# Kernel tuning notes

Hardware: AMD Instinct MI355X
Metric: run time of the kernel (lower is better)

Reference implementation:

```python
import jax, jax.numpy as jnp
import numpy as np

B, L, DIM = 2, 4096, 512
HEADS, KS = 8, 33
HEAD_DIM = DIM // HEADS
SCALE = HEAD_DIM ** -0.5


def setup_inputs() -> dict:
    key = jax.random.key(0)
    ks = jax.random.split(key, 5)
    s = 0.02
    return {
        "x": jax.random.normal(ks[0], (B, L, DIM), dtype=jnp.float32),
        "w_qkv": jax.random.normal(ks[1], (3 * DIM, DIM), dtype=jnp.float32) * s,
        "b_qkv": jax.random.normal(ks[2], (3 * DIM,), dtype=jnp.float32) * s,
        "w_proj": jax.random.normal(ks[3], (DIM, DIM), dtype=jnp.float32) * s,
        "b_proj": jax.random.normal(ks[4], (DIM,), dtype=jnp.float32) * s,
    }


def _na1d(q, k, v):
    # q,k,v: [B, L, H, d]. Each query i attends to KS tokens whose window
    # start is clamp(i - KS//2, 0, L-KS) (NATTEN boundary-clamped neighborhood).
    starts = jnp.clip(jnp.arange(L) - KS // 2, 0, L - KS)          # [L]
    idx = starts[:, None] + jnp.arange(KS)[None, :]                # [L, KS]
    k_g = k[:, idx]                                                # [B, L, KS, H, d]
    v_g = v[:, idx]                                                # [B, L, KS, H, d]
    scores = jnp.einsum("blhd,blkhd->bhlk", q * SCALE, k_g)        # [B, H, L, KS]
    attn = jax.nn.softmax(scores, axis=-1)
    out = jnp.einsum("bhlk,blkhd->blhd", attn, v_g)                # [B, L, H, d]
    return out


def reference(x, w_qkv, b_qkv, w_proj, b_proj):
    qkv = x @ w_qkv.T + b_qkv                                      # [B, L, 3*DIM]
    qkv = qkv.reshape(B, L, 3, HEADS, HEAD_DIM)
    q, k, v = qkv[:, :, 0], qkv[:, :, 1], qkv[:, :, 2]
    out = _na1d(q, k, v).reshape(B, L, DIM)
    return out @ w_proj.T + b_proj
```

## Files before the change

kernel.cpp:

```cpp
#include <hip/hip_runtime.h>
#include <hip/hip_bf16.h>

#define B_ 2
#define L_ 4096
#define DIM_ 512
#define HEADS_ 8
#define HDIM_ 64
#define KS_ 33
#define QKS_ 1024

typedef __bf16 bf16;
typedef __bf16 bf16x4 __attribute__((ext_vector_type(4)));
typedef __bf16 bf16x8 __attribute__((ext_vector_type(8)));
typedef float f32x4 __attribute__((ext_vector_type(4)));

typedef __attribute__((address_space(3))) void lds_void;
typedef __attribute__((address_space(1))) const void glb_void;

__device__ __forceinline__ void async_cp16(const bf16* g, bf16* l)
{
    __builtin_amdgcn_global_load_lds((glb_void*)g, (lds_void*)l, 16, 0, 0);
}

__global__ __launch_bounds__(256)
void cvt_all(const float* __restrict__ x,  const float* __restrict__ wq,
             const float* __restrict__ bq, const float* __restrict__ wp,
             const float* __restrict__ bp,
             bf16* __restrict__ xb,  bf16* __restrict__ wqb,
             bf16* __restrict__ bqb, bf16* __restrict__ wpb,
             bf16* __restrict__ bpb)
{
    const int blk = blockIdx.x;
    const float* src; bf16* dst; int n, base;
    if (blk < 2048)       { src = x;  dst = xb;  n = 4194304; base = blk; }
    else if (blk < 2432)  { src = wq; dst = wqb; n = 786432;  base = blk - 2048; }
    else if (blk < 2560)  { src = wp; dst = wpb; n = 262144;  base = blk - 2432; }
    else if (blk == 2560) { src = bq; dst = bqb; n = 1536;    base = 0; }
    else                  { src = bp; dst = bpb; n = 512;     base = 0; }
    int i = base * 2048 + threadIdx.x * 8;
    if (i + 8 <= n) {
        float4 a = *(const float4*)(src + i);
        float4 b = *(const float4*)(src + i + 4);
        bf16x8 o;
        o[0] = (bf16)a.x; o[1] = (bf16)a.y; o[2] = (bf16)a.z; o[3] = (bf16)a.w;
        o[4] = (bf16)b.x; o[5] = (bf16)b.y; o[6] = (bf16)b.z; o[7] = (bf16)b.w;
        *(bf16x8*)(dst + i) = o;
    }
}

#define GEMM_CORE(A_, W_, K_)                                                  \
    __shared__ bf16 As[128][64];                                               \
    __shared__ bf16 Bs[64][64];                                                \
    const int tid  = threadIdx.x;                                              \
    const int wave = tid >> 6;                                                 \
    const int lane = tid & 63;                                                 \
    const int wm   = (wave >> 1) * 64;                                         \
    const int wn   = (wave & 1) * 32;                                          \
    const int l16  = lane & 15;                                                \
    const int quad = lane >> 4;                                                \
    const int row0 = blockIdx.x * 128;                                         \
    const int col0 = blockIdx.y * 64;                                          \
    f32x4 acc[4][2] = {};                                                      \
    for (int k0 = 0; k0 < (K_); k0 += 64) {                                    \
        _Pragma("unroll")                                                      \
        for (int it = 0; it < 6; ++it) {                                       \
            int f = it * 256 + tid;                                            \
            if (f < 1024) {                                                    \
                int r = f >> 3, pc = f & 7, lc = pc ^ (r & 7);                 \
                async_cp16(&(A_)[(size_t)(row0 + r) * (K_) + k0 + lc * 8],     \
                           &As[r][pc * 8]);                                    \
            } else {                                                           \
                int g = f - 1024;                                              \
                int r = g >> 3, pc = g & 7, lc = pc ^ (r & 7);                 \
                async_cp16(&(W_)[(size_t)(col0 + r) * (K_) + k0 + lc * 8],     \
                           &Bs[r][pc * 8]);                                    \
            }                                                                  \
        }                                                                      \
        __syncthreads();                                                       \
        _Pragma("unroll")                                                      \
        for (int ks = 0; ks < 2; ++ks) {                                       \
            bf16x8 af[4], bfr[2];                                              \
            _Pragma("unroll")                                                  \
            for (int i = 0; i < 4; ++i) {                                      \
                int ra = wm + i * 16 + l16;                                    \
                af[i] = *(const bf16x8*)(&As[ra][((ks * 4 + quad) ^ (ra & 7)) * 8]); \
            }                                                                  \
            _Pragma("unroll")                                                  \
            for (int i = 0; i < 2; ++i) {                                      \
                int rb = wn + i * 16 + l16;                                    \
                bfr[i] = *(const bf16x8*)(&Bs[rb][((ks * 4 + quad) ^ (rb & 7)) * 8]); \
            }                                                                  \
            _Pragma("unroll")                                                  \
            for (int mi = 0; mi < 4; ++mi)                                     \
                _Pragma("unroll")                                              \
                for (int ni = 0; ni < 2; ++ni)                                 \
                    acc[mi][ni] = __builtin_amdgcn_mfma_f32_16x16x32_bf16(     \
                        af[mi], bfr[ni], acc[mi][ni], 0, 0, 0);                \
        }                                                                      \
        __syncthreads();                                                       \
    }

__global__ __launch_bounds__(256)
void gemm_qkv(const bf16* __restrict__ A, const bf16* __restrict__ W,
              const bf16* __restrict__ bias,
              bf16* __restrict__ qk, bf16* __restrict__ vT)
{
    GEMM_CORE(A, W, DIM_)

    if (col0 < 1024) {
        #pragma unroll
        for (int ni = 0; ni < 2; ++ni) {
            int n = col0 + wn + ni * 16 + l16;
            float bv = (float)bias[n];
            #pragma unroll
            for (int mi = 0; mi < 4; ++mi) {
                int mrow = row0 + wm + mi * 16 + quad * 4;
                #pragma unroll
                for (int r = 0; r < 4; ++r)
                    qk[(size_t)(mrow + r) * QKS_ + n] = (bf16)(acc[mi][ni][r] + bv);
            }
        }
    } else {
        #pragma unroll
        for (int ni = 0; ni < 2; ++ni) {
            int nf = col0 + wn + ni * 16 + l16;
            float bv = (float)bias[nf];
            int hd = nf - 1024;
            #pragma unroll
            for (int mi = 0; mi < 4; ++mi) {
                int m = row0 + wm + mi * 16 + quad * 4;
                int b = m >> 12;
                int l = m & (L_ - 1);
                bf16x4 v4;
                #pragma unroll
                for (int r = 0; r < 4; ++r) v4[r] = (bf16)(acc[mi][ni][r] + bv);
                *(bf16x4*)(vT + ((size_t)(b * DIM_ + hd)) * L_ + l) = v4;
            }
        }
    }
}

__global__ __launch_bounds__(256)
void gemm_proj(const bf16* __restrict__ A, const bf16* __restrict__ W,
               const bf16* __restrict__ bias, float* __restrict__ C)
{
    GEMM_CORE(A, W, DIM_)

    #pragma unroll
    for (int ni = 0; ni < 2; ++ni) {
        int n = col0 + wn + ni * 16 + l16;
        float bv = (float)bias[n];
        #pragma unroll
        for (int mi = 0; mi < 4; ++mi) {
            int mrow = row0 + wm + mi * 16 + quad * 4;
            #pragma unroll
            for (int r = 0; r < 4; ++r)
                C[(size_t)(mrow + r) * DIM_ + n] = acc[mi][ni][r] + bv;
        }
    }
}

__global__ __launch_bounds__(256)
void na1d_attn_mfma(const bf16* __restrict__ qk, const bf16* __restrict__ vT,
                    bf16* __restrict__ att)
{
    __shared__ bf16 Klds[96 * 64];
    __shared__ bf16 Plds[4][16][72];

    const int tid  = threadIdx.x;
    const int wave = tid >> 6;
    const int lane = tid & 63;
    const int l16  = lane & 15;
    const int quad = lane >> 4;

    const int xcd  = blockIdx.x & 7;
    const int s    = blockIdx.x >> 3;
    const int jj   = s & 3;
    const int half = (s >> 2) & 1;
    const int h    = (s >> 3) & 7;
    const int b    = s >> 6;
    const int p    = jj * 8 + xcd;
    const int Q0   = p * 128 + half * 64;

    const size_t rowbase = (size_t)b * L_;

    #pragma unroll
    for (int i = 0; i < 3; ++i) {
        int ck = i * 256 + tid;
        int r  = ck >> 3;
        int pc = ck & 7;
        int lc = pc ^ (r & 7);
        int g  = Q0 - 16 + r;
        g = g < 0 ? 0 : (g > L_ - 1 ? L_ - 1 : g);
        async_cp16(qk + (rowbase + g) * QKS_ + DIM_ + h * HDIM_ + lc * 8,
                   Klds + (size_t)ck * 8);
    }

    const int q0w = Q0 + wave * 16;
    const bf16* qptr = qk + (rowbase + q0w + l16) * QKS_ + h * HDIM_ + quad * 8;
    bf16x8 qf0 = *(const bf16x8*)(qptr);
    bf16x8 qf1 = *(const bf16x8*)(qptr + 32);

    int k_base = q0w - 16;
    if (k_base > L_ - 48) k_base = L_ - 48;
    if (k_base < 0) k_base = 0;
    const int rel = k_base - (Q0 - 16);

    __syncthreads();

    f32x4 sacc[3] = {};
    #pragma unroll
    for (int t = 0; t < 3; ++t) {
        int r = rel + t * 16 + l16;
        bf16x8 kf0 = *(const bf16x8*)(Klds + r * 64 + ((quad ^ (r & 7)) * 8));
        bf16x8 kf1 = *(const bf16x8*)(Klds + r * 64 + (((4 + quad) ^ (r & 7)) * 8));
        sacc[t] = __builtin_amdgcn_mfma_f32_16x16x32_bf16(qf0, kf0, sacc[t], 0, 0, 0);
        sacc[t] = __builtin_amdgcn_mfma_f32_16x16x32_bf16(qf1, kf1, sacc[t], 0, 0, 0);
    }

    int offr[4];
    #pragma unroll
    for (int r = 0; r < 4; ++r) {
        int lq = q0w + quad * 4 + r;
        int st = lq - KS_ / 2;
        if (st < 0) st = 0;
        if (st > L_ - KS_) st = L_ - KS_;
        offr[r] = st - k_base;
    }
    float sv[3][4];
    #pragma unroll
    for (int t = 0; t < 3; ++t) {
        int j = t * 16 + l16;
        #pragma unroll
        for (int r = 0; r < 4; ++r) {
            float xv = sacc[t][r] * 0.125f;
            sv[t][r] = (j >= offr[r] && j <= offr[r] + 32) ? xv : -1e30f;
        }
    }

    float mr[4], sum[4];
    #pragma unroll
    for (int r = 0; r < 4; ++r)
        mr[r] = fmaxf(fmaxf(sv[0][r], sv[1][r]), sv[2][r]);
    #pragma unroll
    for (int o = 1; o < 16; o <<= 1)
        #pragma unroll
        for (int r = 0; r < 4; ++r)
            mr[r] = fmaxf(mr[r], __shfl_xor(mr[r], o, 64));
    #pragma unroll
    for (int t = 0; t < 3; ++t)
        #pragma unroll
        for (int r = 0; r < 4; ++r)
            sv[t][r] = __expf(sv[t][r] - mr[r]);
    #pragma unroll
    for (int r = 0; r < 4; ++r)
        sum[r] = sv[0][r] + sv[1][r] + sv[2][r];
    #pragma unroll
    for (int o = 1; o < 16; o <<= 1)
        #pragma unroll
        for (int r = 0; r < 4; ++r)
            sum[r] += __shfl_xor(sum[r], o, 64);
    #pragma unroll
    for (int r = 0; r < 4; ++r) {
        float inv = 1.0f / sum[r];
        #pragma unroll
        for (int t = 0; t < 3; ++t) sv[t][r] *= inv;
    }

    bf16* P = &Plds[wave][0][0];
    {
        int rr = lane >> 2;
        int c0 = 48 + (lane & 3) * 4;
        *(bf16x4*)(&P[rr * 72 + c0]) = (bf16x4){(bf16)0.f, (bf16)0.f, (bf16)0.f, (bf16)0.f};
    }
    #pragma unroll
    for (int t = 0; t < 3; ++t)
        #pragma unroll
        for (int r = 0; r < 4; ++r)
            P[(quad * 4 + r) * 72 + t * 16 + l16] = (bf16)sv[t][r];
    __syncthreads();

    bf16x8 pf0 = *(const bf16x8*)(&P[l16 * 72 + quad * 8]);
    bf16x8 pf1 = *(const bf16x8*)(&P[l16 * 72 + 32 + quad * 8]);

    const bf16* vbase = vT + (size_t)(b * DIM_ + h * HDIM_) * L_;
    int c1 = k_base + quad * 8;
    int c2 = k_base + 32 + quad * 8;
    if (c2 > L_ - 8) c2 = L_ - 8;
    f32x4 o[4] = {};
    #pragma unroll
    for (int t = 0; t < 4; ++t) {
        const bf16* vrow = vbase + (size_t)(t * 16 + l16) * L_;
        bf16x8 vf0 = *(const bf16x8*)(vrow + c1);
        bf16x8 vf1 = *(const bf16x8*)(vrow + c2);
        o[t] = __builtin_amdgcn_mfma_f32_16x16x32_bf16(pf0, vf0, o[t], 0, 0, 0);
        o[t] = __builtin_amdgcn_mfma_f32_16x16x32_bf16(pf1, vf1, o[t], 0, 0, 0);
    }

    bf16* orow = att + (rowbase + q0w) * DIM_ + h * HDIM_;
    #pragma unroll
    for (int t = 0; t < 4; ++t)
        #pragma unroll
        for (int r = 0; r < 4; ++r)
            orow[(size_t)(quad * 4 + r) * DIM_ + t * 16 + l16] = (bf16)o[t][r];
}

extern "C" void kernel_launch(void* const* d_in, const int* in_sizes, int n_in,
                              void* d_out, int out_size, void* d_ws, size_t ws_size,
                              hipStream_t stream) {
    const int n_x  = B_ * L_ * DIM_;
    const int n_wq = 3 * DIM_ * DIM_;
    const int n_bq = 3 * DIM_;
    const int n_wp = DIM_ * DIM_;
    const int n_bp = DIM_;

    char* ws = (char*)d_ws;
    bf16* xb  = (bf16*)ws;
    bf16* wqb = xb  + n_x;
    bf16* bqb = wqb + n_wq;
    bf16* wpb = bqb + n_bq;
    bf16* bpb = wpb + n_wp;
    bf16* qk  = bpb + n_bp;
    bf16* vT  = qk  + (size_t)8192 * 1024;
    bf16* att = vT  + (size_t)B_ * DIM_ * L_;

    float* out = (float*)d_out;
    const int M = B_ * L_;

    cvt_all<<<2562, 256, 0, stream>>>(
        (const float*)d_in[0], (const float*)d_in[1], (const float*)d_in[2],
        (const float*)d_in[3], (const float*)d_in[4],
        xb, wqb, bqb, wpb, bpb);

    gemm_qkv<<<dim3(M / 128, (3 * DIM_) / 64), 256, 0, stream>>>(
        xb, wqb, bqb, qk, vT);

    na1d_attn_mfma<<<dim3((B_ * HEADS_ * L_) / 64), 256, 0, stream>>>(qk, vT, att);

    gemm_proj<<<dim3(M / 128, DIM_ / 64), 256, 0, stream>>>(
        att, wpb, bpb, out);
}
```

Before: 118.0 us.

## Load GEMM fragments directly from global and shrink attention blocks to 32 queries

The GEMM core drops LDS staging and barriers and has each wave load its MFMA fragments straight from global memory, relying on L1/L2 caching for reuse across waves. The attention kernel moves from 64-query, 256-thread blocks to 32-query, 128-thread blocks with a smaller K tile in LDS, doubling the grid. The aim is to cut synchronisation and LDS overhead and raise block count. The cost is more redundant global traffic and uncoalesced 16-byte row loads in the GEMMs, plus more K-halo reloads per query in attention.

```diff
diff --git a/kernel.cpp b/kernel.cpp
--- a/kernel.cpp
+++ b/kernel.cpp
@@ -48,9 +48,7 @@
     }
 }
 
-#define GEMM_CORE(A_, W_, K_)                                                  \
-    __shared__ bf16 As[128][64];                                               \
-    __shared__ bf16 Bs[64][64];                                                \
+#define DGEMM_CORE(A_, W_, K_)                                                 \
     const int tid  = threadIdx.x;                                              \
     const int wave = tid >> 6;                                                 \
     const int lane = tid & 63;                                                 \
@@ -60,44 +58,24 @@
     const int quad = lane >> 4;                                                \
     const int row0 = blockIdx.x * 128;                                         \
     const int col0 = blockIdx.y * 64;                                          \
+    const bf16* Ap = (A_) + (size_t)(row0 + wm + l16) * (K_) + quad * 8;       \
+    const bf16* Wp = (W_) + (size_t)(col0 + wn + l16) * (K_) + quad * 8;       \
     f32x4 acc[4][2] = {};                                                      \
-    for (int k0 = 0; k0 < (K_); k0 += 64) {                                    \
+    _Pragma("unroll 4")                                                        \
+    for (int k = 0; k < (K_); k += 32) {                                       \
+        bf16x8 af[4], bfr[2];                                                  \
         _Pragma("unroll")                                                      \
-        for (int it = 0; it < 6; ++it) {                                       \
-            int f = it * 256 + tid;                                            \
-            if (f < 1024) {                                                    \
-                int r = f >> 3, pc = f & 7, lc = pc ^ (r & 7);                 \
-                async_cp16(&(A_)[(size_t)(row0 + r) * (K_) + k0 + lc * 8],     \
-                           &As[r][pc * 8]);                                    \
-            } else {                                                           \
-                int g = f - 1024;                                              \
-                int r = g >> 3, pc = g & 7, lc = pc ^ (r & 7);                 \
-                async_cp16(&(W_)[(size_t)(col0 + r) * (K_) + k0 + lc * 8],     \
-                           &Bs[r][pc * 8]);                                    \
-            }                                                                  \
-        }                                                                      \
-        __syncthreads();                                                       \
+        for (int i = 0; i < 4; ++i)                                            \
+            af[i] = *(const bf16x8*)(Ap + (size_t)i * 16 * (K_) + k);          \
         _Pragma("unroll")                                                      \
-        for (int ks = 0; ks < 2; ++ks) {                                       \
-            bf16x8 af[4], bfr[2];                                              \
+        for (int i = 0; i < 2; ++i)                                            \
+            bfr[i] = *(const bf16x8*)(Wp + (size_t)i * 16 * (K_) + k);         \
+        _Pragma("unroll")                                                      \
+        for (int mi = 0; mi < 4; ++mi)                                         \
             _Pragma("unroll")                                                  \
-            for (int i = 0; i < 4; ++i) {                                      \
-                int ra = wm + i * 16 + l16;                                    \
-                af[i] = *(const bf16x8*)(&As[ra][((ks * 4 + quad) ^ (ra & 7)) * 8]); \
-            }                                                                  \
-            _Pragma("unroll")                                                  \
-            for (int i = 0; i < 2; ++i) {                                      \
-                int rb = wn + i * 16 + l16;                                    \
-                bfr[i] = *(const bf16x8*)(&Bs[rb][((ks * 4 + quad) ^ (rb & 7)) * 8]); \
-            }                                                                  \
-            _Pragma("unroll")                                                  \
-            for (int mi = 0; mi < 4; ++mi)                                     \
-                _Pragma("unroll")                                              \
-                for (int ni = 0; ni < 2; ++ni)                                 \
-                    acc[mi][ni] = __builtin_amdgcn_mfma_f32_16x16x32_bf16(     \
-                        af[mi], bfr[ni], acc[mi][ni], 0, 0, 0);                \
-        }                                                                      \
-        __syncthreads();                                                       \
+            for (int ni = 0; ni < 2; ++ni)                                     \
+                acc[mi][ni] = __builtin_amdgcn_mfma_f32_16x16x32_bf16(         \
+                    af[mi], bfr[ni], acc[mi][ni], 0, 0, 0);                    \
     }
 
 __global__ __launch_bounds__(256)
@@ -105,7 +83,7 @@
               const bf16* __restrict__ bias,
               bf16* __restrict__ qk, bf16* __restrict__ vT)
 {
-    GEMM_CORE(A, W, DIM_)
+    DGEMM_CORE(A, W, DIM_)
 
     if (col0 < 1024) {
         #pragma unroll
@@ -144,7 +122,7 @@
 void gemm_proj(const bf16* __restrict__ A, const bf16* __restrict__ W,
                const bf16* __restrict__ bias, float* __restrict__ C)
 {
-    GEMM_CORE(A, W, DIM_)
+    DGEMM_CORE(A, W, DIM_)
 
     #pragma unroll
     for (int ni = 0; ni < 2; ++ni) {
@@ -160,12 +138,12 @@
     }
 }
 
-__global__ __launch_bounds__(256)
+__global__ __launch_bounds__(128)
 void na1d_attn_mfma(const bf16* __restrict__ qk, const bf16* __restrict__ vT,
                     bf16* __restrict__ att)
 {
-    __shared__ bf16 Klds[96 * 64];
-    __shared__ bf16 Plds[4][16][72];
+    __shared__ bf16 Klds[64 * 64];
+    __shared__ bf16 Plds[2][16][72];
 
     const int tid  = threadIdx.x;
     const int wave = tid >> 6;
@@ -175,18 +153,18 @@
 
     const int xcd  = blockIdx.x & 7;
     const int s    = blockIdx.x >> 3;
-    const int jj   = s & 3;
-    const int half = (s >> 2) & 1;
-    const int h    = (s >> 3) & 7;
-    const int b    = s >> 6;
+    const int qtr  = s & 3;
+    const int jj   = (s >> 2) & 3;
+    const int h    = (s >> 4) & 7;
+    const int b    = s >> 7;
     const int p    = jj * 8 + xcd;
-    const int Q0   = p * 128 + half * 64;
+    const int Q0   = p * 128 + qtr * 32;
 
     const size_t rowbase = (size_t)b * L_;
 
     #pragma unroll
-    for (int i = 0; i < 3; ++i) {
-        int ck = i * 256 + tid;
+    for (int i = 0; i < 4; ++i) {
+        int ck = i * 128 + tid;
         int r  = ck >> 3;
         int pc = ck & 7;
         int lc = pc ^ (r & 7);
@@ -335,7 +313,7 @@
     gemm_qkv<<<dim3(M / 128, (3 * DIM_) / 64), 256, 0, stream>>>(
         xb, wqb, bqb, qk, vT);
 
-    na1d_attn_mfma<<<dim3((B_ * HEADS_ * L_) / 64), 256, 0, stream>>>(qk, vT, att);
+    na1d_attn_mfma<<<dim3((B_ * HEADS_ * L_) / 32), 128, 0, stream>>>(qk, vT, att);
 
     gemm_proj<<<dim3(M / 128, DIM_ / 64), 256, 0, stream>>>(
         att, wpb, bpb, out);
```

Measured after the change: 190.7 us. 1.62x slower.
